# Optimization experiments

Hardware: AMD Instinct MI355X
Metric: run time of the kernel (lower is better)

Reference implementation:

```python
import jax, jax.numpy as jnp
import numpy as np

N_LAYERS = 2
D_MODEL = 256
N_STATE = 16


def _rmsnorm(x):
    eps = jnp.finfo(x.dtype).eps
    return x * jax.lax.rsqrt(jnp.mean(x * x, axis=-1, keepdims=True) + eps)


def _selective_scan(x, A, W_delta, b_delta, W_B, W_C, D_skip):
    # x: [B, L, D]; A: [D, N] (negative diagonal); W_delta: [D, D]; W_B/W_C: [D, N]
    dt = jax.nn.softplus(jnp.einsum('bld,de->ble', x, W_delta) + b_delta)  # [B,L,D]
    Bm = jnp.einsum('bld,dn->bln', x, W_B)  # [B,L,N]
    Cm = jnp.einsum('bld,dn->bln', x, W_C)  # [B,L,N]
    # ZOH-style discretization: h_t = a_t * h_{t-1} + b_t
    a = jnp.exp(dt[..., None] * A)                              # [B,L,D,N]
    b = dt[..., None] * Bm[:, :, None, :] * x[..., None]        # [B,L,D,N]

    def combine(c1, c2):
        a1, b1 = c1
        a2, b2 = c2
        return a1 * a2, a2 * b1 + b2

    _, h = jax.lax.associative_scan(combine, (a, b), axis=1)    # [B,L,D,N]
    y = jnp.einsum('bldn,bln->bld', h, Cm) + D_skip * x
    return y


def setup_inputs() -> dict:
    key = jax.random.key(0)
    ks = jax.random.split(key, 9)
    B, L, D, N, NL = 2, 4096, D_MODEL, N_STATE, N_LAYERS
    x = jax.random.normal(ks[0], (B, L, D), dtype=jnp.float32)
    # negative real diagonal A (real_random=False baseline init, kept strictly negative)
    A = -(jax.random.uniform(ks[1], (NL, D, N), dtype=jnp.float32) + 0.5)
    sd = 1.0 / np.sqrt(D)
    W_delta = jax.random.normal(ks[2], (NL, D, D), dtype=jnp.float32) * sd
    b_delta = jnp.zeros((NL, D), dtype=jnp.float32)
    W_B = jax.random.normal(ks[3], (NL, D, N), dtype=jnp.float32) * sd
    W_C = jax.random.normal(ks[4], (NL, D, N), dtype=jnp.float32) * sd
    D_skip = jnp.ones((NL, D), dtype=jnp.float32)
    W_mix = jax.random.normal(ks[5], (NL, D, D), dtype=jnp.float32) * sd
    b_mix = jnp.zeros((NL, D), dtype=jnp.float32)
    return {"x": x, "A": A, "W_delta": W_delta, "b_delta": b_delta,
            "W_B": W_B, "W_C": W_C, "D_skip": D_skip,
            "W_mix": W_mix, "b_mix": b_mix}


def reference(x, A, W_delta, b_delta, W_B, W_C, D_skip, W_mix, b_mix):
    h = x
    for l in range(N_LAYERS):
        h = _rmsnorm(h)                                        # RMSNorm (no affine)
        h = _selective_scan(h, A[l], W_delta[l], b_delta[l],
                            W_B[l], W_C[l], D_skip[l])         # S6Block
        h = jax.nn.gelu(h)                                     # activation
        h = jnp.einsum('bld,de->ble', h, W_mix[l]) + b_mix[l]  # MixingBlock
    return _rmsnorm(h)                                          # final RMSNorm
```

## Files before the change

### kernel.cpp

```cpp
#include <hip/hip_runtime.h>
#include <hip/hip_bf16.h>

#define BATCH 2
#define LSEQ 4096
#define DM 256
#define NS 16
#define BL (BATCH*LSEQ)
#define CHUNK 32
#define NCHUNK (LSEQ/CHUNK)
#define NCHAIN (BATCH*DM*NS)
#define SEG 8
#define CPS (NCHUNK/SEG)
#define MS_STRIDE 260
#define LOG2E 1.4426950408889634f

typedef _Float16 f16x8 __attribute__((ext_vector_type(8)));
typedef _Float16 f16x4 __attribute__((ext_vector_type(4)));
typedef float f32x4 __attribute__((ext_vector_type(4)));

__device__ __forceinline__ float softplus_f(float z){
    return fmaxf(z, 0.0f) + log1pf(__expf(-fabsf(z)));
}
__device__ __forceinline__ float gelu_f(float x){
    float u = 0.7978845608028654f*(x + 0.044715f*x*x*x);
    float e = __builtin_amdgcn_exp2f(2.0f*LOG2E*u);
    float th = 1.0f - 2.0f*__builtin_amdgcn_rcpf(e + 1.0f);
    return 0.5f*x*(1.0f + th);
}

__global__ __launch_bounds__(256) void pack_w_k(const float* __restrict__ Wd,
                         const float* __restrict__ WB,
                         const float* __restrict__ WC,
                         const float* __restrict__ Wm,
                         _Float16* __restrict__ pd0, _Float16* __restrict__ pm0,
                         _Float16* __restrict__ pd1, _Float16* __restrict__ pm1){
    int cfg = blockIdx.y;
    int layer = cfg >> 1;
    int isMix = cfg & 1;
    int count = isMix ? 16*8*64 : 18*8*64;
    int t = blockIdx.x*256 + threadIdx.x;
    if (t >= count) return;
    int lane = t & 63;
    int ks   = (t >> 6) & 7;
    int nt16 = t >> 9;
    int col  = nt16*16 + (lane & 15);
    int kb   = ks*32 + ((lane >> 4) << 3);
    const float* Wd_l = Wd + (size_t)layer*DM*DM;
    const float* WB_l = WB + (size_t)layer*DM*NS;
    const float* WC_l = WC + (size_t)layer*DM*NS;
    const float* Wm_l = Wm + (size_t)layer*DM*DM;
    f16x8 v;
    #pragma unroll
    for (int i=0;i<8;++i){
        float s;
        if (isMix)          s = Wm_l[(size_t)(kb+i)*DM + col];
        else if (col < 256) s = Wd_l[(size_t)(kb+i)*DM + col];
        else if (col < 272) s = WB_l[(size_t)(kb+i)*NS + (col-256)];
        else                s = WC_l[(size_t)(kb+i)*NS + (col-272)];
        v[i] = (_Float16)s;
    }
    _Float16* dst = isMix ? (layer ? pm1 : pm0) : (layer ? pd1 : pd0);
    ((f16x8*)dst)[t] = v;
}

__global__ __launch_bounds__(576) void fused_pre(const float* __restrict__ xin,
                          const _Float16* __restrict__ wp,
                          const float* __restrict__ bd,
                          float* __restrict__ xn,
                          float* __restrict__ dt,
                          float* __restrict__ Bm,
                          float* __restrict__ Cm){
    __shared__ _Float16 xs[32*32*8];
    int t = threadIdx.x;
    int row0 = blockIdx.x*32;
    if (t < 512){
        int r = t >> 4;
        int cb = t & 15;
        const float4* src = (const float4*)(xin + (size_t)(row0+r)*DM);
        float4 v[4];
        float ss = 0.0f;
        #pragma unroll
        for (int j=0;j<4;++j){
            v[j] = src[cb + 16*j];
            ss += v[j].x*v[j].x + v[j].y*v[j].y + v[j].z*v[j].z + v[j].w*v[j].w;
        }
        ss += __shfl_xor(ss, 1, 64);
        ss += __shfl_xor(ss, 2, 64);
        ss += __shfl_xor(ss, 4, 64);
        ss += __shfl_xor(ss, 8, 64);
        float s = rsqrtf(ss*(1.0f/DM) + 1.1920929e-07f);
        float4* xout = (float4*)(xn + (size_t)(row0+r)*DM);
        #pragma unroll
        for (int j=0;j<4;++j){
            int c4 = cb + 16*j;
            float4 o; o.x=v[j].x*s; o.y=v[j].y*s; o.z=v[j].z*s; o.w=v[j].w*s;
            xout[c4] = o;
            int slot = c4 >> 1;
            int j0   = (c4 & 1)*4;
            f16x4 hv; hv[0]=(_Float16)o.x; hv[1]=(_Float16)o.y;
            hv[2]=(_Float16)o.z; hv[3]=(_Float16)o.w;
            *(f16x4*)&xs[((size_t)r*32 + (slot ^ (r & 7)))*8 + j0] = hv;
        }
    }
    __syncthreads();
    int w    = t >> 6;
    int lane = t & 63;
    const f16x8* wpb = (const f16x8*)wp;
    int rl = lane & 15;
    int kg = lane >> 4;
    f32x4 acc[2][2] = {};
    #pragma unroll
    for (int ks=0; ks<8; ++ks){
        int s0 = kg + ks*4;
        f16x8 a0 = *(const f16x8*)&xs[((size_t)(rl     )*32 + (s0 ^ (rl & 7)))*8];
        f16x8 a1 = *(const f16x8*)&xs[((size_t)(rl + 16)*32 + (s0 ^ (rl & 7)))*8];
        f16x8 b0 = wpb[((w*2    )*8 + ks)*64 + lane];
        f16x8 b1 = wpb[((w*2 + 1)*8 + ks)*64 + lane];
        acc[0][0] = __builtin_amdgcn_mfma_f32_16x16x32_f16(a0,b0,acc[0][0],0,0,0);
        acc[0][1] = __builtin_amdgcn_mfma_f32_16x16x32_f16(a0,b1,acc[0][1],0,0,0);
        acc[1][0] = __builtin_amdgcn_mfma_f32_16x16x32_f16(a1,b0,acc[1][0],0,0,0);
        acc[1][1] = __builtin_amdgcn_mfma_f32_16x16x32_f16(a1,b1,acc[1][1],0,0,0);
    }
    int c0 = w*32 + (lane & 15);
    int rb = row0 + ((lane >> 4) << 2);
    if (w < 8){
        float bias0 = bd[c0], bias1 = bd[c0 + 16];
        #pragma unroll
        for (int mi=0; mi<2; ++mi){
            #pragma unroll
            for (int r=0; r<4; ++r){
                int grow = rb + mi*16 + r;
                dt[(size_t)grow*DM + c0]      = softplus_f(acc[mi][0][r] + bias0);
                dt[(size_t)grow*DM + c0 + 16] = softplus_f(acc[mi][1][r] + bias1);
            }
        }
    } else {
        int n = lane & 15;
        #pragma unroll
        for (int mi=0; mi<2; ++mi){
            #pragma unroll
            for (int r=0; r<4; ++r){
                int grow = rb + mi*16 + r;
                Bm[(size_t)grow*NS + n] = acc[mi][0][r];
                Cm[(size_t)grow*NS + n] = acc[mi][1][r];
            }
        }
    }
}

__global__ __launch_bounds__(576) void fused_mid(const _Float16* __restrict__ yh,
                          const _Float16* __restrict__ wpm,
                          const float* __restrict__ bm,
                          const _Float16* __restrict__ wpd,
                          const float* __restrict__ bd,
                          float* __restrict__ xn,
                          float* __restrict__ dt,
                          float* __restrict__ Bm,
                          float* __restrict__ Cm){
    __shared__ float ms[32*MS_STRIDE];
    __shared__ _Float16 xs[32*32*8];
    int t = threadIdx.x;
    int w = t >> 6, lane = t & 63;
    int row0 = blockIdx.x*32;
    if (w < 8){
        const f16x8* ah  = (const f16x8*)yh;
        const f16x8* wpb = (const f16x8*)wpm;
        size_t a0i = (size_t)(row0 + (lane & 15))*32 + (lane >> 4);
        f32x4 acc[2][2] = {};
        #pragma unroll
        for (int ks=0; ks<8; ++ks){
            f16x8 a0 = ah[a0i + ks*4];
            f16x8 a1 = ah[a0i + 512 + ks*4];
            f16x8 b0 = wpb[((w*2    )*8 + ks)*64 + lane];
            f16x8 b1 = wpb[((w*2 + 1)*8 + ks)*64 + lane];
            acc[0][0] = __builtin_amdgcn_mfma_f32_16x16x32_f16(a0,b0,acc[0][0],0,0,0);
            acc[0][1] = __builtin_amdgcn_mfma_f32_16x16x32_f16(a0,b1,acc[0][1],0,0,0);
            acc[1][0] = __builtin_amdgcn_mfma_f32_16x16x32_f16(a1,b0,acc[1][0],0,0,0);
            acc[1][1] = __builtin_amdgcn_mfma_f32_16x16x32_f16(a1,b1,acc[1][1],0,0,0);
        }
        int c0 = w*32 + (lane & 15);
        int rb = (lane >> 4) << 2;
        float bias0 = bm[c0], bias1 = bm[c0 + 16];
        #pragma unroll
        for (int mi=0; mi<2; ++mi){
            #pragma unroll
            for (int r=0; r<4; ++r){
                int lr = rb + mi*16 + r;
                ms[lr*MS_STRIDE + c0]      = acc[mi][0][r] + bias0;
                ms[lr*MS_STRIDE + c0 + 16] = acc[mi][1][r] + bias1;
            }
        }
    }
    __syncthreads();
    if (t < 512){
        int r = t >> 4;
        int cb = t & 15;
        float4 v[4];
        float ss = 0.0f;
        #pragma unroll
        for (int j=0;j<4;++j){
            v[j] = *(const float4*)&ms[r*MS_STRIDE + (cb + 16*j)*4];
            ss += v[j].x*v[j].x + v[j].y*v[j].y + v[j].z*v[j].z + v[j].w*v[j].w;
        }
        ss += __shfl_xor(ss, 1, 64);
        ss += __shfl_xor(ss, 2, 64);
        ss += __shfl_xor(ss, 4, 64);
        ss += __shfl_xor(ss, 8, 64);
        float s = rsqrtf(ss*(1.0f/DM) + 1.1920929e-07f);
        float4* xout = (float4*)(xn + (size_t)(row0+r)*DM);
        #pragma unroll
        for (int j=0;j<4;++j){
            int c4 = cb + 16*j;
            float4 o; o.x=v[j].x*s; o.y=v[j].y*s; o.z=v[j].z*s; o.w=v[j].w*s;
            xout[c4] = o;
            int slot = c4 >> 1;
            int j0   = (c4 & 1)*4;
            f16x4 hv; hv[0]=(_Float16)o.x; hv[1]=(_Float16)o.y;
            hv[2]=(_Float16)o.z; hv[3]=(_Float16)o.w;
            *(f16x4*)&xs[((size_t)r*32 + (slot ^ (r & 7)))*8 + j0] = hv;
        }
    }
    __syncthreads();
    {
        const f16x8* wpb = (const f16x8*)wpd;
        int rl = lane & 15;
        int kg = lane >> 4;
        f32x4 acc[2][2] = {};
        #pragma unroll
        for (int ks=0; ks<8; ++ks){
            int s0 = kg + ks*4;
            f16x8 a0 = *(const f16x8*)&xs[((size_t)(rl     )*32 + (s0 ^ (rl & 7)))*8];
            f16x8 a1 = *(const f16x8*)&xs[((size_t)(rl + 16)*32 + (s0 ^ (rl & 7)))*8];
            f16x8 b0 = wpb[((w*2    )*8 + ks)*64 + lane];
            f16x8 b1 = wpb[((w*2 + 1)*8 + ks)*64 + lane];
            acc[0][0] = __builtin_amdgcn_mfma_f32_16x16x32_f16(a0,b0,acc[0][0],0,0,0);
            acc[0][1] = __builtin_amdgcn_mfma_f32_16x16x32_f16(a0,b1,acc[0][1],0,0,0);
            acc[1][0] = __builtin_amdgcn_mfma_f32_16x16x32_f16(a1,b0,acc[1][0],0,0,0);
            acc[1][1] = __builtin_amdgcn_mfma_f32_16x16x32_f16(a1,b1,acc[1][1],0,0,0);
        }
        int c0 = w*32 + (lane & 15);
        int rb = row0 + ((lane >> 4) << 2);
        if (w < 8){
            float bias0 = bd[c0], bias1 = bd[c0 + 16];
            #pragma unroll
            for (int mi=0; mi<2; ++mi){
                #pragma unroll
                for (int r=0; r<4; ++r){
                    int grow = rb + mi*16 + r;
                    dt[(size_t)grow*DM + c0]      = softplus_f(acc[mi][0][r] + bias0);
                    dt[(size_t)grow*DM + c0 + 16] = softplus_f(acc[mi][1][r] + bias1);
                }
            }
        } else {
            int n = lane & 15;
            #pragma unroll
            for (int mi=0; mi<2; ++mi){
                #pragma unroll
                for (int r=0; r<4; ++r){
                    int grow = rb + mi*16 + r;
                    Bm[(size_t)grow*NS + n] = acc[mi][0][r];
                    Cm[(size_t)grow*NS + n] = acc[mi][1][r];
                }
            }
        }
    }
}

__global__ __launch_bounds__(512) void fused_out(const _Float16* __restrict__ yh,
                          const _Float16* __restrict__ wpm,
                          const float* __restrict__ bm,
                          float* __restrict__ out){
    __shared__ float ms[32*MS_STRIDE];
    int t = threadIdx.x;
    int w = t >> 6, lane = t & 63;
    int row0 = blockIdx.x*32;
    {
        const f16x8* ah  = (const f16x8*)yh;
        const f16x8* wpb = (const f16x8*)wpm;
        size_t a0i = (size_t)(row0 + (lane & 15))*32 + (lane >> 4);
        f32x4 acc[2][2] = {};
        #pragma unroll
        for (int ks=0; ks<8; ++ks){
            f16x8 a0 = ah[a0i + ks*4];
            f16x8 a1 = ah[a0i + 512 + ks*4];
            f16x8 b0 = wpb[((w*2    )*8 + ks)*64 + lane];
            f16x8 b1 = wpb[((w*2 + 1)*8 + ks)*64 + lane];
            acc[0][0] = __builtin_amdgcn_mfma_f32_16x16x32_f16(a0,b0,acc[0][0],0,0,0);
            acc[0][1] = __builtin_amdgcn_mfma_f32_16x16x32_f16(a0,b1,acc[0][1],0,0,0);
            acc[1][0] = __builtin_amdgcn_mfma_f32_16x16x32_f16(a1,b0,acc[1][0],0,0,0);
            acc[1][1] = __builtin_amdgcn_mfma_f32_16x16x32_f16(a1,b1,acc[1][1],0,0,0);
        }
        int c0 = w*32 + (lane & 15);
        int rb = (lane >> 4) << 2;
        float bias0 = bm[c0], bias1 = bm[c0 + 16];
        #pragma unroll
        for (int mi=0; mi<2; ++mi){
            #pragma unroll
            for (int r=0; r<4; ++r){
                int lr = rb + mi*16 + r;
                ms[lr*MS_STRIDE + c0]      = acc[mi][0][r] + bias0;
                ms[lr*MS_STRIDE + c0 + 16] = acc[mi][1][r] + bias1;
            }
        }
    }
    __syncthreads();
    {
        int r = t >> 4;
        int cb = t & 15;
        float4 v[4];
        float ss = 0.0f;
        #pragma unroll
        for (int j=0;j<4;++j){
            v[j] = *(const float4*)&ms[r*MS_STRIDE + (cb + 16*j)*4];
            ss += v[j].x*v[j].x + v[j].y*v[j].y + v[j].z*v[j].z + v[j].w*v[j].w;
        }
        ss += __shfl_xor(ss, 1, 64);
        ss += __shfl_xor(ss, 2, 64);
        ss += __shfl_xor(ss, 4, 64);
        ss += __shfl_xor(ss, 8, 64);
        float s = rsqrtf(ss*(1.0f/DM) + 1.1920929e-07f);
        float4* xout = (float4*)(out + (size_t)(row0+r)*DM);
        #pragma unroll
        for (int j=0;j<4;++j){
            float4 o = v[j];
            o.x*=s; o.y*=s; o.z*=s; o.w*=s;
            xout[cb + 16*j] = o;
        }
    }
}

__global__ __launch_bounds__(256) void scan_p1(const float* __restrict__ xn,
                        const float* __restrict__ dt,
                        const float* __restrict__ Bmv,
                        const float* __restrict__ A,
                        float* __restrict__ cA, float* __restrict__ cB){
    __shared__ float4 bs[CHUNK*4];
    int tid = threadIdx.x;
    int c = blockIdx.x, dq = blockIdx.y, b = blockIdx.z;
    int dl = tid >> 2, nq = tid & 3;
    int d  = dq*64 + dl;
    int row0 = b*LSEQ + c*CHUNK;
    if (tid < CHUNK*4) bs[tid] = ((const float4*)(Bmv + (size_t)row0*NS))[tid];
    float4 Alg = ((const float4*)(A + (size_t)d*NS))[nq];
    Alg.x *= LOG2E; Alg.y *= LOG2E; Alg.z *= LOG2E; Alg.w *= LOG2E;
    __syncthreads();
    float Ap0=1,Ap1=1,Ap2=1,Ap3=1, Bp0=0,Bp1=0,Bp2=0,Bp3=0;
    #pragma unroll 4
    for (int tt=0; tt<CHUNK; ++tt){
        float dtv = dt[(size_t)(row0+tt)*DM + d];
        float xv  = xn[(size_t)(row0+tt)*DM + d];
        float dtx = dtv*xv;
        float4 bq = bs[tt*4 + nq];
        float a0 = __builtin_amdgcn_exp2f(dtv*Alg.x);
        float a1 = __builtin_amdgcn_exp2f(dtv*Alg.y);
        float a2 = __builtin_amdgcn_exp2f(dtv*Alg.z);
        float a3 = __builtin_amdgcn_exp2f(dtv*Alg.w);
        Ap0 *= a0; Bp0 = fmaf(a0, Bp0, dtx*bq.x);
        Ap1 *= a1; Bp1 = fmaf(a1, Bp1, dtx*bq.y);
        Ap2 *= a2; Bp2 = fmaf(a2, Bp2, dtx*bq.z);
        Ap3 *= a3; Bp3 = fmaf(a3, Bp3, dtx*bq.w);
    }
    size_t base = (size_t)c*NCHAIN + ((size_t)b*DM + d)*NS + nq*4;
    *(float4*)(cA + base) = make_float4(Ap0,Ap1,Ap2,Ap3);
    *(float4*)(cB + base) = make_float4(Bp0,Bp1,Bp2,Bp3);
}

__global__ __launch_bounds__(256) void scan_p2(const float* __restrict__ cA,
                        const float* __restrict__ cB,
                        float* __restrict__ hin){
    int gt = blockIdx.x*256 + threadIdx.x;
    int chain = gt >> 3;
    int seg   = gt & 7;
    int c0 = seg*CPS;
    float Ac = 1.0f, Bc = 0.0f;
    #pragma unroll 4
    for (int i=0;i<CPS;++i){
        size_t idx = (size_t)(c0+i)*NCHAIN + chain;
        float a = cA[idx], b = cB[idx];
        Bc = fmaf(a, Bc, b);
        Ac *= a;
    }
    #pragma unroll
    for (int dlt=1; dlt<8; dlt<<=1){
        float Apv = __shfl_up(Ac, dlt, 64);
        float Bpv = __shfl_up(Bc, dlt, 64);
        if (seg >= dlt){
            Bc = fmaf(Ac, Bpv, Bc);
            Ac *= Apv;
        }
    }
    float hprev = __shfl_up(Bc, 1, 64);
    float h = (seg == 0) ? 0.0f : hprev;
    #pragma unroll 4
    for (int i=0;i<CPS;++i){
        size_t idx = (size_t)(c0+i)*NCHAIN + chain;
        hin[idx] = h;
        h = fmaf(cA[idx], h, cB[idx]);
    }
}

__global__ __launch_bounds__(256) void scan_p3(const float* __restrict__ xn,
                        const float* __restrict__ dt,
                        const float* __restrict__ Bmv,
                        const float* __restrict__ Cmv,
                        const float* __restrict__ A,
                        const float* __restrict__ Dsk,
                        const float* __restrict__ hin,
                        _Float16* __restrict__ yh){
    __shared__ float4 bs[CHUNK*4], cs[CHUNK*4];
    int tid = threadIdx.x;
    int c = blockIdx.x, dq = blockIdx.y, b = blockIdx.z;
    int dl = tid >> 2, nq = tid & 3;
    int d  = dq*64 + dl;
    int row0 = b*LSEQ + c*CHUNK;
    if (tid < CHUNK*4){
        bs[tid] = ((const float4*)(Bmv + (size_t)row0*NS))[tid];
        cs[tid] = ((const float4*)(Cmv + (size_t)row0*NS))[tid];
    }
    float4 Alg = ((const float4*)(A + (size_t)d*NS))[nq];
    Alg.x *= LOG2E; Alg.y *= LOG2E; Alg.z *= LOG2E; Alg.w *= LOG2E;
    float dsk = Dsk[d];
    float4 hv = ((const float4*)(hin + (size_t)c*NCHAIN + ((size_t)b*DM + d)*NS))[nq];
    float h0=hv.x, h1=hv.y, h2=hv.z, h3=hv.w;
    __syncthreads();
    #pragma unroll 4
    for (int tt=0; tt<CHUNK; ++tt){
        float dtv = dt[(size_t)(row0+tt)*DM + d];
        float xv  = xn[(size_t)(row0+tt)*DM + d];
        float dtx = dtv*xv;
        float4 bq = bs[tt*4 + nq];
        float4 cq = cs[tt*4 + nq];
        float a0 = __builtin_amdgcn_exp2f(dtv*Alg.x);
        float a1 = __builtin_amdgcn_exp2f(dtv*Alg.y);
        float a2 = __builtin_amdgcn_exp2f(dtv*Alg.z);
        float a3 = __builtin_amdgcn_exp2f(dtv*Alg.w);
        h0 = fmaf(a0, h0, dtx*bq.x);
        h1 = fmaf(a1, h1, dtx*bq.y);
        h2 = fmaf(a2, h2, dtx*bq.z);
        h3 = fmaf(a3, h3, dtx*bq.w);
        float p = fmaf(h0, cq.x, fmaf(h1, cq.y, fmaf(h2, cq.z, h3*cq.w)));
        p += __shfl_xor(p, 1, 64);
        p += __shfl_xor(p, 2, 64);
        if (nq == 0){
            float yv = p + dsk*xv;
            yh[(size_t)(row0+tt)*DM + d] = (_Float16)gelu_f(yv);
        }
    }
}

extern "C" void kernel_launch(void* const* d_in, const int* in_sizes, int n_in,
                              void* d_out, int out_size, void* d_ws, size_t ws_size,
                              hipStream_t stream) {
    const float* x  = (const float*)d_in[0];
    const float* A  = (const float*)d_in[1];
    const float* Wd = (const float*)d_in[2];
    const float* bd = (const float*)d_in[3];
    const float* WB = (const float*)d_in[4];
    const float* WC = (const float*)d_in[5];
    const float* Ds = (const float*)d_in[6];
    const float* Wm = (const float*)d_in[7];
    const float* bm = (const float*)d_in[8];
    float* out = (float*)d_out;

    const size_t BSZ = (size_t)BL*DM;
    const size_t CH  = (size_t)NCHUNK*NCHAIN;
    float* ws  = (float*)d_ws;
    float* b0  = ws;
    float* b1  = b0  + BSZ;
    float* b2  = b1  + BSZ;
    float* Bmb = b2  + BSZ;
    float* Cmb = Bmb + (size_t)BL*NS;
    float* cA  = Cmb + (size_t)BL*NS;
    float* cB  = cA  + CH;
    float* hin = cB  + CH;
    _Float16* packs = (_Float16*)(hin + CH);
    _Float16* pd0 = packs;
    _Float16* pd1 = pd0 + 73728;
    _Float16* pm0 = pd1 + 73728;
    _Float16* pm1 = pm0 + 65536;
    _Float16* yh = (_Float16*)cB;

    dim3 gscan(NCHUNK, DM/64, BATCH);

    pack_w_k<<<dim3(36,4), 256, 0, stream>>>(Wd, WB, WC, Wm, pd0, pm0, pd1, pm1);

    const float* A1  = A  + (size_t)DM*NS;
    const float* bd1 = bd + DM;
    const float* Ds1 = Ds + DM;
    const float* bm1 = bm + DM;

    fused_pre<<<BL/32, 576, 0, stream>>>(x, pd0, bd, b0, b1, Bmb, Cmb);
    scan_p1<<<gscan, 256, 0, stream>>>(b0, b1, Bmb, A, cA, cB);
    scan_p2<<<NCHAIN*SEG/256, 256, 0, stream>>>(cA, cB, hin);
    scan_p3<<<gscan, 256, 0, stream>>>(b0, b1, Bmb, Cmb, A, Ds, hin, yh);
    fused_mid<<<BL/32, 576, 0, stream>>>(yh, pm0, bm, pd1, bd1, b0, b1, Bmb, Cmb);
    scan_p1<<<gscan, 256, 0, stream>>>(b0, b1, Bmb, A1, cA, cB);
    scan_p2<<<NCHAIN*SEG/256, 256, 0, stream>>>(cA, cB, hin);
    scan_p3<<<gscan, 256, 0, stream>>>(b0, b1, Bmb, Cmb, A1, Ds1, hin, yh);
    fused_out<<<BL/32, 512, 0, stream>>>(yh, pm1, bm1, out);
}
```

Baseline: 182.4 us.

## Fuse chunk-summary scan pass into projection kernels and stage scan_p3 inputs in LDS

The first pass of the chunked scan (per-chunk products of a and accumulated b) is folded into the projection kernels. Those kernels already hold dt, x and B for the 32-row chunk in shared memory, so the separate scan_p1 launch and its re-read of dt/xn/Bm from global memory go away. The summary runs on 512 threads, each handling 8 states for one channel. scan_p3 now loads its dt and xn tile into LDS with coalesced float4 loads instead of strided per-timestep global reads, and yh moves to its own workspace region. In exchange, the projection kernels use more shared memory and run longer, which may lower occupancy.

```diff
diff --git a/kernel.cpp b/kernel.cpp
--- a/kernel.cpp
+++ b/kernel.cpp
@@ -11,7 +11,7 @@
 #define NCHAIN (BATCH*DM*NS)
 #define SEG 8
 #define CPS (NCHUNK/SEG)
-#define MS_STRIDE 260
+#define SUM_STRIDE 264
 #define LOG2E 1.4426950408889634f
 
 typedef _Float16 f16x8 __attribute__((ext_vector_type(8)));
@@ -63,16 +63,64 @@
     ((f16x8*)dst)[t] = v;
 }
 
-__global__ __launch_bounds__(576) void fused_pre(const float* __restrict__ xin,
+__device__ __forceinline__ void chunk_summary(const float* buf,
+                    const _Float16* xs, const float* bsm,
+                    const float* __restrict__ A,
+                    float* __restrict__ cA, float* __restrict__ cB,
+                    int b, int c, int t){
+    if (t >= 512) return;
+    int ng = t >> 8;
+    int d  = t & 255;
+    float Alg[8];
+    {
+        const float4* ap = (const float4*)(A + (size_t)d*NS + ng*8);
+        float4 a0 = ap[0], a1 = ap[1];
+        Alg[0]=a0.x*LOG2E; Alg[1]=a0.y*LOG2E; Alg[2]=a0.z*LOG2E; Alg[3]=a0.w*LOG2E;
+        Alg[4]=a1.x*LOG2E; Alg[5]=a1.y*LOG2E; Alg[6]=a1.z*LOG2E; Alg[7]=a1.w*LOG2E;
+    }
+    float Ap[8], Bp[8];
+    #pragma unroll
+    for (int j=0;j<8;++j){ Ap[j]=1.0f; Bp[j]=0.0f; }
+    int xsl = d >> 3, xel = d & 7;
+    #pragma unroll 4
+    for (int tt=0; tt<CHUNK; ++tt){
+        float dtv = buf[tt*SUM_STRIDE + d];
+        float xv  = (float)xs[((size_t)tt*32 + (xsl ^ (tt & 7)))*8 + xel];
+        float dtx = dtv*xv;
+        const float4* bp4 = (const float4*)&bsm[tt*16 + ng*8];
+        float4 b0 = bp4[0], b1 = bp4[1];
+        float bv[8] = {b0.x,b0.y,b0.z,b0.w,b1.x,b1.y,b1.z,b1.w};
+        #pragma unroll
+        for (int j=0;j<8;++j){
+            float a = __builtin_amdgcn_exp2f(dtv*Alg[j]);
+            Ap[j] *= a;
+            Bp[j] = fmaf(a, Bp[j], dtx*bv[j]);
+        }
+    }
+    size_t base = (size_t)c*NCHAIN + ((size_t)b*DM + d)*NS + ng*8;
+    *(float4*)(cA + base)     = make_float4(Ap[0],Ap[1],Ap[2],Ap[3]);
+    *(float4*)(cA + base + 4) = make_float4(Ap[4],Ap[5],Ap[6],Ap[7]);
+    *(float4*)(cB + base)     = make_float4(Bp[0],Bp[1],Bp[2],Bp[3]);
+    *(float4*)(cB + base + 4) = make_float4(Bp[4],Bp[5],Bp[6],Bp[7]);
+}
+
+__global__ __launch_bounds__(576) void fused_pre_s(const float* __restrict__ xin,
                           const _Float16* __restrict__ wp,
                           const float* __restrict__ bd,
+                          const float* __restrict__ A,
                           float* __restrict__ xn,
                           float* __restrict__ dt,
                           float* __restrict__ Bm,
-                          float* __restrict__ Cm){
+                          float* __restrict__ Cm,
+                          float* __restrict__ cA,
+                          float* __restrict__ cB){
+    __shared__ float buf[32*SUM_STRIDE];
     __shared__ _Float16 xs[32*32*8];
+    __shared__ float bsm[32*16];
     int t = threadIdx.x;
     int row0 = blockIdx.x*32;
+    int b = row0 >> 12;
+    int c = (row0 & (LSEQ-1)) >> 5;
     if (t < 512){
         int r = t >> 4;
         int cb = t & 15;
@@ -105,124 +153,8 @@
     __syncthreads();
     int w    = t >> 6;
     int lane = t & 63;
-    const f16x8* wpb = (const f16x8*)wp;
-    int rl = lane & 15;
-    int kg = lane >> 4;
-    f32x4 acc[2][2] = {};
-    #pragma unroll
-    for (int ks=0; ks<8; ++ks){
-        int s0 = kg + ks*4;
-        f16x8 a0 = *(const f16x8*)&xs[((size_t)(rl     )*32 + (s0 ^ (rl & 7)))*8];
-        f16x8 a1 = *(const f16x8*)&xs[((size_t)(rl + 16)*32 + (s0 ^ (rl & 7)))*8];
-        f16x8 b0 = wpb[((w*2    )*8 + ks)*64 + lane];
-        f16x8 b1 = wpb[((w*2 + 1)*8 + ks)*64 + lane];
-        acc[0][0] = __builtin_amdgcn_mfma_f32_16x16x32_f16(a0,b0,acc[0][0],0,0,0);
-        acc[0][1] = __builtin_amdgcn_mfma_f32_16x16x32_f16(a0,b1,acc[0][1],0,0,0);
-        acc[1][0] = __builtin_amdgcn_mfma_f32_16x16x32_f16(a1,b0,acc[1][0],0,0,0);
-        acc[1][1] = __builtin_amdgcn_mfma_f32_16x16x32_f16(a1,b1,acc[1][1],0,0,0);
-    }
-    int c0 = w*32 + (lane & 15);
-    int rb = row0 + ((lane >> 4) << 2);
-    if (w < 8){
-        float bias0 = bd[c0], bias1 = bd[c0 + 16];
-        #pragma unroll
-        for (int mi=0; mi<2; ++mi){
-            #pragma unroll
-            for (int r=0; r<4; ++r){
-                int grow = rb + mi*16 + r;
-                dt[(size_t)grow*DM + c0]      = softplus_f(acc[mi][0][r] + bias0);
-                dt[(size_t)grow*DM + c0 + 16] = softplus_f(acc[mi][1][r] + bias1);
-            }
-        }
-    } else {
-        int n = lane & 15;
-        #pragma unroll
-        for (int mi=0; mi<2; ++mi){
-            #pragma unroll
-            for (int r=0; r<4; ++r){
-                int grow = rb + mi*16 + r;
-                Bm[(size_t)grow*NS + n] = acc[mi][0][r];
-                Cm[(size_t)grow*NS + n] = acc[mi][1][r];
-            }
-        }
-    }
-}
-
-__global__ __launch_bounds__(576) void fused_mid(const _Float16* __restrict__ yh,
-                          const _Float16* __restrict__ wpm,
-                          const float* __restrict__ bm,
-                          const _Float16* __restrict__ wpd,
-                          const float* __restrict__ bd,
-                          float* __restrict__ xn,
-                          float* __restrict__ dt,
-                          float* __restrict__ Bm,
-                          float* __restrict__ Cm){
-    __shared__ float ms[32*MS_STRIDE];
-    __shared__ _Float16 xs[32*32*8];
-    int t = threadIdx.x;
-    int w = t >> 6, lane = t & 63;
-    int row0 = blockIdx.x*32;
-    if (w < 8){
-        const f16x8* ah  = (const f16x8*)yh;
-        const f16x8* wpb = (const f16x8*)wpm;
-        size_t a0i = (size_t)(row0 + (lane & 15))*32 + (lane >> 4);
-        f32x4 acc[2][2] = {};
-        #pragma unroll
-        for (int ks=0; ks<8; ++ks){
-            f16x8 a0 = ah[a0i + ks*4];
-            f16x8 a1 = ah[a0i + 512 + ks*4];
-            f16x8 b0 = wpb[((w*2    )*8 + ks)*64 + lane];
-            f16x8 b1 = wpb[((w*2 + 1)*8 + ks)*64 + lane];
-            acc[0][0] = __builtin_amdgcn_mfma_f32_16x16x32_f16(a0,b0,acc[0][0],0,0,0);
-            acc[0][1] = __builtin_amdgcn_mfma_f32_16x16x32_f16(a0,b1,acc[0][1],0,0,0);
-            acc[1][0] = __builtin_amdgcn_mfma_f32_16x16x32_f16(a1,b0,acc[1][0],0,0,0);
-            acc[1][1] = __builtin_amdgcn_mfma_f32_16x16x32_f16(a1,b1,acc[1][1],0,0,0);
-        }
-        int c0 = w*32 + (lane & 15);
-        int rb = (lane >> 4) << 2;
-        float bias0 = bm[c0], bias1 = bm[c0 + 16];
-        #pragma unroll
-        for (int mi=0; mi<2; ++mi){
-            #pragma unroll
-            for (int r=0; r<4; ++r){
-                int lr = rb + mi*16 + r;
-                ms[lr*MS_STRIDE + c0]      = acc[mi][0][r] + bias0;
-                ms[lr*MS_STRIDE + c0 + 16] = acc[mi][1][r] + bias1;
-            }
-        }
-    }
-    __syncthreads();
-    if (t < 512){
-        int r = t >> 4;
-        int cb = t & 15;
-        float4 v[4];
-        float ss = 0.0f;
-        #pragma unroll
-        for (int j=0;j<4;++j){
-            v[j] = *(const float4*)&ms[r*MS_STRIDE + (cb + 16*j)*4];
-            ss += v[j].x*v[j].x + v[j].y*v[j].y + v[j].z*v[j].z + v[j].w*v[j].w;
-        }
-        ss += __shfl_xor(ss, 1, 64);
-        ss += __shfl_xor(ss, 2, 64);
-        ss += __shfl_xor(ss, 4, 64);
-        ss += __shfl_xor(ss, 8, 64);
-        float s = rsqrtf(ss*(1.0f/DM) + 1.1920929e-07f);
-        float4* xout = (float4*)(xn + (size_t)(row0+r)*DM);
-        #pragma unroll
-        for (int j=0;j<4;++j){
-            int c4 = cb + 16*j;
-            float4 o; o.x=v[j].x*s; o.y=v[j].y*s; o.z=v[j].z*s; o.w=v[j].w*s;
-            xout[c4] = o;
-            int slot = c4 >> 1;
-            int j0   = (c4 & 1)*4;
-            f16x4 hv; hv[0]=(_Float16)o.x; hv[1]=(_Float16)o.y;
-            hv[2]=(_Float16)o.z; hv[3]=(_Float16)o.w;
-            *(f16x4*)&xs[((size_t)r*32 + (slot ^ (r & 7)))*8 + j0] = hv;
-        }
-    }
-    __syncthreads();
     {
-        const f16x8* wpb = (const f16x8*)wpd;
+        const f16x8* wpb = (const f16x8*)wp;
         int rl = lane & 15;
         int kg = lane >> 4;
         f32x4 acc[2][2] = {};
@@ -239,16 +171,21 @@
             acc[1][1] = __builtin_amdgcn_mfma_f32_16x16x32_f16(a1,b1,acc[1][1],0,0,0);
         }
         int c0 = w*32 + (lane & 15);
-        int rb = row0 + ((lane >> 4) << 2);
+        int lrb = (lane >> 4) << 2;
         if (w < 8){
             float bias0 = bd[c0], bias1 = bd[c0 + 16];
             #pragma unroll
             for (int mi=0; mi<2; ++mi){
                 #pragma unroll
                 for (int r=0; r<4; ++r){
-                    int grow = rb + mi*16 + r;
-                    dt[(size_t)grow*DM + c0]      = softplus_f(acc[mi][0][r] + bias0);
-                    dt[(size_t)grow*DM + c0 + 16] = softplus_f(acc[mi][1][r] + bias1);
+                    int lr = lrb + mi*16 + r;
+                    int grow = row0 + lr;
+                    float v0 = softplus_f(acc[mi][0][r] + bias0);
+                    float v1 = softplus_f(acc[mi][1][r] + bias1);
+                    dt[(size_t)grow*DM + c0]      = v0;
+                    dt[(size_t)grow*DM + c0 + 16] = v1;
+                    buf[lr*SUM_STRIDE + c0]      = v0;
+                    buf[lr*SUM_STRIDE + c0 + 16] = v1;
                 }
             }
         } else {
@@ -257,24 +194,40 @@
             for (int mi=0; mi<2; ++mi){
                 #pragma unroll
                 for (int r=0; r<4; ++r){
-                    int grow = rb + mi*16 + r;
+                    int lr = lrb + mi*16 + r;
+                    int grow = row0 + lr;
                     Bm[(size_t)grow*NS + n] = acc[mi][0][r];
                     Cm[(size_t)grow*NS + n] = acc[mi][1][r];
+                    bsm[lr*16 + n] = acc[mi][0][r];
                 }
             }
         }
     }
-}
-
-__global__ __launch_bounds__(512) void fused_out(const _Float16* __restrict__ yh,
+    __syncthreads();
+    chunk_summary(buf, xs, bsm, A, cA, cB, b, c, t);
+}
+
+__global__ __launch_bounds__(576) void fused_mid_s(const _Float16* __restrict__ yh,
                           const _Float16* __restrict__ wpm,
                           const float* __restrict__ bm,
-                          float* __restrict__ out){
-    __shared__ float ms[32*MS_STRIDE];
+                          const _Float16* __restrict__ wpd,
+                          const float* __restrict__ bd,
+                          const float* __restrict__ A,
+                          float* __restrict__ xn,
+                          float* __restrict__ dt,
+                          float* __restrict__ Bm,
+                          float* __restrict__ Cm,
+                          float* __restrict__ cA,
+                          float* __restrict__ cB){
+    __shared__ float buf[32*SUM_STRIDE];
+    __shared__ _Float16 xs[32*32*8];
+    __shared__ float bsm[32*16];
     int t = threadIdx.x;
     int w = t >> 6, lane = t & 63;
     int row0 = blockIdx.x*32;
-    {
+    int b = row0 >> 12;
+    int c = (row0 & (LSEQ-1)) >> 5;
+    if (w < 8){
         const f16x8* ah  = (const f16x8*)yh;
         const f16x8* wpb = (const f16x8*)wpm;
         size_t a0i = (size_t)(row0 + (lane & 15))*32 + (lane >> 4);
@@ -291,15 +244,136 @@
             acc[1][1] = __builtin_amdgcn_mfma_f32_16x16x32_f16(a1,b1,acc[1][1],0,0,0);
         }
         int c0 = w*32 + (lane & 15);
-        int rb = (lane >> 4) << 2;
+        int lrb = (lane >> 4) << 2;
         float bias0 = bm[c0], bias1 = bm[c0 + 16];
         #pragma unroll
         for (int mi=0; mi<2; ++mi){
             #pragma unroll
             for (int r=0; r<4; ++r){
-                int lr = rb + mi*16 + r;
-                ms[lr*MS_STRIDE + c0]      = acc[mi][0][r] + bias0;
-                ms[lr*MS_STRIDE + c0 + 16] = acc[mi][1][r] + bias1;
+                int lr = lrb + mi*16 + r;
+                buf[lr*SUM_STRIDE + c0]      = acc[mi][0][r] + bias0;
+                buf[lr*SUM_STRIDE + c0 + 16] = acc[mi][1][r] + bias1;
+            }
+        }
+    }
+    __syncthreads();
+    if (t < 512){
+        int r = t >> 4;
+        int cb = t & 15;
+        float4 v[4];
+        float ss = 0.0f;
+        #pragma unroll
+        for (int j=0;j<4;++j){
+            v[j] = *(const float4*)&buf[r*SUM_STRIDE + (cb + 16*j)*4];
+            ss += v[j].x*v[j].x + v[j].y*v[j].y + v[j].z*v[j].z + v[j].w*v[j].w;
+        }
+        ss += __shfl_xor(ss, 1, 64);
+        ss += __shfl_xor(ss, 2, 64);
+        ss += __shfl_xor(ss, 4, 64);
+        ss += __shfl_xor(ss, 8, 64);
+        float s = rsqrtf(ss*(1.0f/DM) + 1.1920929e-07f);
+        float4* xout = (float4*)(xn + (size_t)(row0+r)*DM);
+        #pragma unroll
+        for (int j=0;j<4;++j){
+            int c4 = cb + 16*j;
+            float4 o; o.x=v[j].x*s; o.y=v[j].y*s; o.z=v[j].z*s; o.w=v[j].w*s;
+            xout[c4] = o;
+            int slot = c4 >> 1;
+            int j0   = (c4 & 1)*4;
+            f16x4 hv; hv[0]=(_Float16)o.x; hv[1]=(_Float16)o.y;
+            hv[2]=(_Float16)o.z; hv[3]=(_Float16)o.w;
+            *(f16x4*)&xs[((size_t)r*32 + (slot ^ (r & 7)))*8 + j0] = hv;
+        }
+    }
+    __syncthreads();
+    {
+        const f16x8* wpb = (const f16x8*)wpd;
+        int rl = lane & 15;
+        int kg = lane >> 4;
+        f32x4 acc[2][2] = {};
+        #pragma unroll
+        for (int ks=0; ks<8; ++ks){
+            int s0 = kg + ks*4;
+            f16x8 a0 = *(const f16x8*)&xs[((size_t)(rl     )*32 + (s0 ^ (rl & 7)))*8];
+            f16x8 a1 = *(const f16x8*)&xs[((size_t)(rl + 16)*32 + (s0 ^ (rl & 7)))*8];
+            f16x8 b0 = wpb[((w*2    )*8 + ks)*64 + lane];
+            f16x8 b1 = wpb[((w*2 + 1)*8 + ks)*64 + lane];
+            acc[0][0] = __builtin_amdgcn_mfma_f32_16x16x32_f16(a0,b0,acc[0][0],0,0,0);
+            acc[0][1] = __builtin_amdgcn_mfma_f32_16x16x32_f16(a0,b1,acc[0][1],0,0,0);
+            acc[1][0] = __builtin_amdgcn_mfma_f32_16x16x32_f16(a1,b0,acc[1][0],0,0,0);
+            acc[1][1] = __builtin_amdgcn_mfma_f32_16x16x32_f16(a1,b1,acc[1][1],0,0,0);
+        }
+        int c0 = w*32 + (lane & 15);
+        int lrb = (lane >> 4) << 2;
+        if (w < 8){
+            float bias0 = bd[c0], bias1 = bd[c0 + 16];
+            #pragma unroll
+            for (int mi=0; mi<2; ++mi){
+                #pragma unroll
+                for (int r=0; r<4; ++r){
+                    int lr = lrb + mi*16 + r;
+                    int grow = row0 + lr;
+                    float v0 = softplus_f(acc[mi][0][r] + bias0);
+                    float v1 = softplus_f(acc[mi][1][r] + bias1);
+                    dt[(size_t)grow*DM + c0]      = v0;
+                    dt[(size_t)grow*DM + c0 + 16] = v1;
+                    buf[lr*SUM_STRIDE + c0]      = v0;
+                    buf[lr*SUM_STRIDE + c0 + 16] = v1;
+                }
+            }
+        } else {
+            int n = lane & 15;
+            #pragma unroll
+            for (int mi=0; mi<2; ++mi){
+                #pragma unroll
+                for (int r=0; r<4; ++r){
+                    int lr = lrb + mi*16 + r;
+                    int grow = row0 + lr;
+                    Bm[(size_t)grow*NS + n] = acc[mi][0][r];
+                    Cm[(size_t)grow*NS + n] = acc[mi][1][r];
+                    bsm[lr*16 + n] = acc[mi][0][r];
+                }
+            }
+        }
+    }
+    __syncthreads();
+    chunk_summary(buf, xs, bsm, A, cA, cB, b, c, t);
+}
+
+__global__ __launch_bounds__(512) void fused_out(const _Float16* __restrict__ yh,
+                          const _Float16* __restrict__ wpm,
+                          const float* __restrict__ bm,
+                          float* __restrict__ out){
+    __shared__ float ms[32*SUM_STRIDE];
+    int t = threadIdx.x;
+    int w = t >> 6, lane = t & 63;
+    int row0 = blockIdx.x*32;
+    {
+        const f16x8* ah  = (const f16x8*)yh;
+        const f16x8* wpb = (const f16x8*)wpm;
+        size_t a0i = (size_t)(row0 + (lane & 15))*32 + (lane >> 4);
+        f32x4 acc[2][2] = {};
+        #pragma unroll
+        for (int ks=0; ks<8; ++ks){
+            f16x8 a0 = ah[a0i + ks*4];
+            f16x8 a1 = ah[a0i + 512 + ks*4];
+            f16x8 b0 = wpb[((w*2    )*8 + ks)*64 + lane];
+            f16x8 b1 = wpb[((w*2 + 1)*8 + ks)*64 + lane];
+            acc[0][0] = __builtin_amdgcn_mfma_f32_16x16x32_f16(a0,b0,acc[0][0],0,0,0);
+            acc[0][1] = __builtin_amdgcn_mfma_f32_16x16x32_f16(a0,b1,acc[0][1],0,0,0);
+            acc[1][0] = __builtin_amdgcn_mfma_f32_16x16x32_f16(a1,b0,acc[1][0],0,0,0);
+            acc[1][1] = __builtin_amdgcn_mfma_f32_16x16x32_f16(a1,b1,acc[1][1],0,0,0);
+        }
+        int c0 = w*32 + (lane & 15);
+        int lrb = (lane >> 4) << 2;
+        float bias0 = bm[c0], bias1 = bm[c0 + 16];
+        #pragma unroll
+        for (int mi=0; mi<2; ++mi){
+            #pragma unroll
+            for (int r=0; r<4; ++r){
+                int lr = lrb + mi*16 + r;
+                ms[lr*SUM_STRIDE + c0]      = acc[mi][0][r] + bias0;
+                ms[lr*SUM_STRIDE + c0 + 16] = acc[mi][1][r] + bias1;
             }
         }
     }
@@ -311,7 +385,7 @@
         float ss = 0.0f;
         #pragma unroll
         for (int j=0;j<4;++j){
-            v[j] = *(const float4*)&ms[r*MS_STRIDE + (cb + 16*j)*4];
+            v[j] = *(const float4*)&ms[r*SUM_STRIDE + (cb + 16*j)*4];
             ss += v[j].x*v[j].x + v[j].y*v[j].y + v[j].z*v[j].z + v[j].w*v[j].w;
         }
         ss += __shfl_xor(ss, 1, 64);
@@ -327,42 +401,6 @@
             xout[cb + 16*j] = o;
         }
     }
-}
-
-__global__ __launch_bounds__(256) void scan_p1(const float* __restrict__ xn,
-                        const float* __restrict__ dt,
-                        const float* __restrict__ Bmv,
-                        const float* __restrict__ A,
-                        float* __restrict__ cA, float* __restrict__ cB){
-    __shared__ float4 bs[CHUNK*4];
-    int tid = threadIdx.x;
-    int c = blockIdx.x, dq = blockIdx.y, b = blockIdx.z;
-    int dl = tid >> 2, nq = tid & 3;
-    int d  = dq*64 + dl;
-    int row0 = b*LSEQ + c*CHUNK;
-    if (tid < CHUNK*4) bs[tid] = ((const float4*)(Bmv + (size_t)row0*NS))[tid];
-    float4 Alg = ((const float4*)(A + (size_t)d*NS))[nq];
-    Alg.x *= LOG2E; Alg.y *= LOG2E; Alg.z *= LOG2E; Alg.w *= LOG2E;
-    __syncthreads();
-    float Ap0=1,Ap1=1,Ap2=1,Ap3=1, Bp0=0,Bp1=0,Bp2=0,Bp3=0;
-    #pragma unroll 4
-    for (int tt=0; tt<CHUNK; ++tt){
-        float dtv = dt[(size_t)(row0+tt)*DM + d];
-        float xv  = xn[(size_t)(row0+tt)*DM + d];
-        float dtx = dtv*xv;
-        float4 bq = bs[tt*4 + nq];
-        float a0 = __builtin_amdgcn_exp2f(dtv*Alg.x);
-        float a1 = __builtin_amdgcn_exp2f(dtv*Alg.y);
-        float a2 = __builtin_amdgcn_exp2f(dtv*Alg.z);
-        float a3 = __builtin_amdgcn_exp2f(dtv*Alg.w);
-        Ap0 *= a0; Bp0 = fmaf(a0, Bp0, dtx*bq.x);
-        Ap1 *= a1; Bp1 = fmaf(a1, Bp1, dtx*bq.y);
-        Ap2 *= a2; Bp2 = fmaf(a2, Bp2, dtx*bq.z);
-        Ap3 *= a3; Bp3 = fmaf(a3, Bp3, dtx*bq.w);
-    }
-    size_t base = (size_t)c*NCHAIN + ((size_t)b*DM + d)*NS + nq*4;
-    *(float4*)(cA + base) = make_float4(Ap0,Ap1,Ap2,Ap3);
-    *(float4*)(cB + base) = make_float4(Bp0,Bp1,Bp2,Bp3);
 }
 
 __global__ __launch_bounds__(256) void scan_p2(const float* __restrict__ cA,
@@ -407,12 +445,22 @@
                         const float* __restrict__ Dsk,
                         const float* __restrict__ hin,
                         _Float16* __restrict__ yh){
+    __shared__ float sdt[CHUNK][64];
+    __shared__ float sxn[CHUNK][64];
     __shared__ float4 bs[CHUNK*4], cs[CHUNK*4];
     int tid = threadIdx.x;
     int c = blockIdx.x, dq = blockIdx.y, b = blockIdx.z;
     int dl = tid >> 2, nq = tid & 3;
     int d  = dq*64 + dl;
     int row0 = b*LSEQ + c*CHUNK;
+    {
+        int t0 = tid >> 4, cg = tid & 15;
+        *(float4*)&sdt[t0][cg*4] = *(const float4*)(dt + (size_t)(row0+t0)*DM + dq*64 + cg*4);
+        *(float4*)&sxn[t0][cg*4] = *(const float4*)(xn + (size_t)(row0+t0)*DM + dq*64 + cg*4);
+        int t1 = t0 + 16;
+        *(float4*)&sdt[t1][cg*4] = *(const float4*)(dt + (size_t)(row0+t1)*DM + dq*64 + cg*4);
+        *(float4*)&sxn[t1][cg*4] = *(const float4*)(xn + (size_t)(row0+t1)*DM + dq*64 + cg*4);
+    }
     if (tid < CHUNK*4){
         bs[tid] = ((const float4*)(Bmv + (size_t)row0*NS))[tid];
         cs[tid] = ((const float4*)(Cmv + (size_t)row0*NS))[tid];
@@ -425,8 +473,8 @@
     __syncthreads();
     #pragma unroll 4
     for (int tt=0; tt<CHUNK; ++tt){
-        float dtv = dt[(size_t)(row0+tt)*DM + d];
-        float xv  = xn[(size_t)(row0+tt)*DM + d];
+        float dtv = sdt[tt][dl];
+        float xv  = sxn[tt][dl];
         float dtx = dtv*xv;
         float4 bq = bs[tt*4 + nq];
         float4 cq = cs[tt*4 + nq];
@@ -467,8 +515,7 @@
     float* ws  = (float*)d_ws;
     float* b0  = ws;
     float* b1  = b0  + BSZ;
-    float* b2  = b1  + BSZ;
-    float* Bmb = b2  + BSZ;
+    float* Bmb = b1  + BSZ;
     float* Cmb = Bmb + (size_t)BL*NS;
     float* cA  = Cmb + (size_t)BL*NS;
     float* cB  = cA  + CH;
@@ -478,7 +525,7 @@
     _Float16* pd1 = pd0 + 73728;
     _Float16* pm0 = pd1 + 73728;
     _Float16* pm1 = pm0 + 65536;
-    _Float16* yh = (_Float16*)cB;
+    _Float16* yh  = pm1 + 65536;
 
     dim3 gscan(NCHUNK, DM/64, BATCH);
 
@@ -489,12 +536,11 @@
     const float* Ds1 = Ds + DM;
     const float* bm1 = bm + DM;
 
-    fused_pre<<<BL/32, 576, 0, stream>>>(x, pd0, bd, b0, b1, Bmb, Cmb);
-    scan_p1<<<gscan, 256, 0, stream>>>(b0, b1, Bmb, A, cA, cB);
+    fused_pre_s<<<BL/32, 576, 0, stream>>>(x, pd0, bd, A, b0, b1, Bmb, Cmb, cA, cB);
     scan_p2<<<NCHAIN*SEG/256, 256, 0, stream>>>(cA, cB, hin);
     scan_p3<<<gscan, 256, 0, stream>>>(b0, b1, Bmb, Cmb, A, Ds, hin, yh);
-    fused_mid<<<BL/32, 576, 0, stream>>>(yh, pm0, bm, pd1, bd1, b0, b1, Bmb, Cmb);
-    scan_p1<<<gscan, 256, 0, stream>>>(b0, b1, Bmb, A1, cA, cB);
+    fused_mid_s<<<BL/32, 576, 0, stream>>>(yh, pm0, bm, pd1, bd1, A1,
+                                           b0, b1, Bmb, Cmb, cA, cB);
     scan_p2<<<NCHAIN*SEG/256, 256, 0, stream>>>(cA, cB, hin);
     scan_p3<<<gscan, 256, 0, stream>>>(b0, b1, Bmb, Cmb, A1, Ds1, hin, yh);
     fused_out<<<BL/32, 512, 0, stream>>>(yh, pm1, bm1, out);
```

Result: faster. 171.2 us (-6.1%).
